# Kernel optimization log

Hardware: AMD Instinct MI355X
Metric: run time of the kernel (lower is better)

The kernel has to match this reference:

```python
import jax, jax.numpy as jnp
import numpy as np

# ---- config mirrored from FullyFusedNGP.__init__ (scale=1) ----
SCALE = 1.0
L, F, LOG2_T, N_MIN = 16, 2, 19, 16
T = 1 << LOG2_T  # 524288 entries per level
B = float(np.exp(np.log(2048.0 * SCALE / N_MIN) / (L - 1)))  # per_level_scale
RES = np.array([int(np.ceil(N_MIN * B**l - 1.0)) + 1 for l in range(L)], dtype=np.int32)
PRIMES = np.array([1, 2654435761, 805459861], dtype=np.uint32)  # tcnn hash primes
CORNERS = np.array([[(i >> k) & 1 for k in range(3)] for i in range(8)], dtype=np.int32)  # [8,3]
N_PTS = 262144


def hash_encode(xn, table):
    """Multi-resolution hash grid with trilinear interpolation.
    xn: [N,3] in [0,1]; table: [L,T,F] -> returns [N, L*F]."""
    res = jnp.asarray(RES)
    corners = jnp.asarray(CORNERS)
    pos = xn[None] * (res[:, None, None] - 1).astype(xn.dtype)        # [L,N,3]
    p0 = jnp.floor(pos).astype(jnp.int32)
    w = pos - p0                                                      # [L,N,3] trilinear fracs
    idx = p0[:, :, None, :] + corners[None, None]                     # [L,N,8,3]
    idx = jnp.clip(idx, 0, (res - 1)[:, None, None, None])
    ui = idx.astype(jnp.uint32)
    h = (ui[..., 0] * PRIMES[0]) ^ (ui[..., 1] * PRIMES[1]) ^ (ui[..., 2] * PRIMES[2])
    h = (h & jnp.uint32(T - 1)).astype(jnp.int32)                     # [L,N,8]
    feats = jax.vmap(lambda t, hh: t[hh])(table, h)                   # [L,N,8,F] gather
    cw = jnp.where(corners[None, None].astype(bool),
                   w[:, :, None, :], 1.0 - w[:, :, None, :]).prod(-1)  # [L,N,8]
    feat = (feats * cw[..., None]).sum(2)                             # [L,N,F]
    return jnp.moveaxis(feat, 0, 1).reshape(xn.shape[0], L * F)       # [N,32]


def sh_encode(d01):
    """Spherical harmonics degree 4 (tcnn convention, input in [0,1]). [N,3]->[N,16]."""
    d = 2.0 * d01 - 1.0
    x, y, z = d[:, 0], d[:, 1], d[:, 2]
    xy, xz, yz = x * y, x * z, y * z
    x2, y2, z2 = x * x, y * y, z * z
    return jnp.stack([
        jnp.full_like(x, 0.28209479177387814),
        -0.48860251190291987 * y,
        0.48860251190291987 * z,
        -0.48860251190291987 * x,
        1.0925484305920792 * xy,
        -1.0925484305920792 * yz,
        0.94617469575755997 * z2 - 0.31539156525251999,
        -1.0925484305920792 * xz,
        0.54627421529603959 * (x2 - y2),
        0.59004358992664352 * y * (-3.0 * x2 + y2),
        2.8906114426405538 * xy * z,
        0.45704579946446572 * y * (1.0 - 5.0 * z2),
        0.3731763325901154 * z * (5.0 * z2 - 3.0),
        0.45704579946446572 * x * (1.0 - 5.0 * z2),
        1.4453057213202769 * z * (x2 - y2),
        0.59004358992664352 * x * (-x2 + 3.0 * y2),
    ], axis=1)


def setup_inputs() -> dict:
    key = jax.random.key(0)
    ks = jax.random.split(key, 8)
    x = jax.random.uniform(ks[0], (N_PTS, 3), jnp.float32, -SCALE, SCALE)
    d = jax.random.normal(ks[1], (N_PTS, 3), jnp.float32)
    d = d / jnp.linalg.norm(d, axis=1, keepdims=True)
    table = jax.random.uniform(ks[2], (L, T, F), jnp.float32, -1e-4, 1e-4)
    def w(k, fi, fo):  # bias-free FullyFusedMLP weights
        return jax.random.normal(k, (fi, fo), jnp.float32) * (1.0 / np.sqrt(fi))
    return {
        'x': x, 'd': d, 'table': table,
        'w1': w(ks[3], 32, 64), 'w2': w(ks[4], 64, 16),
        'w_in': w(ks[5], 32, 64), 'w_h': w(ks[6], 64, 64), 'w_out': w(ks[7], 64, 3),
    }


def reference(x, d, table, w1, w2, w_in, w_h, w_out):
    xn = (x + SCALE) / (2.0 * SCALE)                 # (x - xyz_min)/(xyz_max - xyz_min)
    enc = hash_encode(xn, table)                     # [N,32]
    h = jax.nn.relu(enc @ w1) @ w2                   # density MLP, 1 hidden layer -> [N,16]
    sigmas = jnp.exp(h[:, 0])                        # TruncExp forward == exp
    sh = sh_encode((d + 1.0) * 0.5)                  # [N,16]
    a = jax.nn.relu(jnp.concatenate([sh, h], axis=1) @ w_in)
    a = jax.nn.relu(a @ w_h)
    rgbs = jax.nn.sigmoid(a @ w_out)                 # [N,3]
    return sigmas, rgbs
```

## Files before the change

kernel.cpp:

```cpp
#include <hip/hip_runtime.h>
#include <hip/hip_bf16.h>
#include <stdint.h>

typedef __bf16 bf16x8 __attribute__((ext_vector_type(8)));
typedef float  f32x4  __attribute__((ext_vector_type(4)));

__device__ __forceinline__ int imin(int a, int b) { return a < b ? a : b; }
__device__ __forceinline__ int imax(int a, int b) { return a > b ? a : b; }

#define TMASK ((1u << 19) - 1u)

__constant__ int cRES[16] = {16, 23, 31, 43, 59, 81, 112, 154,
                             213, 295, 407, 562, 777, 1073, 1483, 2048};

__global__ void __launch_bounds__(256) ngp_encode(
    const float* __restrict__ xin,
    const float2* __restrict__ tab,
    float2* __restrict__ enc,
    int n, int lbase)
{
    const int bid = blockIdx.x;
    const int l = lbase + (bid & 7);
    const int p = (bid >> 3) * 256 + threadIdx.x;
    if (p >= n) return;

    const int rm = cRES[l] - 1;
    const float rf = (float)rm;

    const float xn0 = (xin[3 * p + 0] + 1.0f) * 0.5f;
    const float xn1 = (xin[3 * p + 1] + 1.0f) * 0.5f;
    const float xn2 = (xin[3 * p + 2] + 1.0f) * 0.5f;

    const float p0 = xn0 * rf, p1 = xn1 * rf, p2 = xn2 * rf;
    const float f0 = floorf(p0), f1 = floorf(p1), f2 = floorf(p2);
    const int i0 = (int)f0, i1 = (int)f1, i2 = (int)f2;
    const float w0 = p0 - f0, w1 = p1 - f1, w2 = p2 - f2;

    const int a0 = imax(imin(i0, rm), 0), b0 = imax(imin(i0 + 1, rm), 0);
    const int a1 = imax(imin(i1, rm), 0), b1 = imax(imin(i1 + 1, rm), 0);
    const int a2 = imax(imin(i2, rm), 0), b2 = imax(imin(i2 + 1, rm), 0);

    const uint32_t t0a = (uint32_t)a0;
    const uint32_t t0b = (uint32_t)b0;
    const uint32_t t1a = (uint32_t)a1 * 2654435761u;
    const uint32_t t1b = (uint32_t)b1 * 2654435761u;
    const uint32_t t2a = (uint32_t)a2 * 805459861u;
    const uint32_t t2b = (uint32_t)b2 * 805459861u;
    const uint32_t base = (uint32_t)l << 19;

    const float2 v000 = tab[base + ((t0a ^ t1a ^ t2a) & TMASK)];
    const float2 v100 = tab[base + ((t0b ^ t1a ^ t2a) & TMASK)];
    const float2 v010 = tab[base + ((t0a ^ t1b ^ t2a) & TMASK)];
    const float2 v110 = tab[base + ((t0b ^ t1b ^ t2a) & TMASK)];
    const float2 v001 = tab[base + ((t0a ^ t1a ^ t2b) & TMASK)];
    const float2 v101 = tab[base + ((t0b ^ t1a ^ t2b) & TMASK)];
    const float2 v011 = tab[base + ((t0a ^ t1b ^ t2b) & TMASK)];
    const float2 v111 = tab[base + ((t0b ^ t1b ^ t2b) & TMASK)];

    const float u0 = 1.0f - w0, u1 = 1.0f - w1, u2 = 1.0f - w2;
    float e0 = 0.0f, e1 = 0.0f;
    {   float cw = u0 * u1 * u2;  e0 = fmaf(v000.x, cw, e0); e1 = fmaf(v000.y, cw, e1); }
    {   float cw = w0 * u1 * u2;  e0 = fmaf(v100.x, cw, e0); e1 = fmaf(v100.y, cw, e1); }
    {   float cw = u0 * w1 * u2;  e0 = fmaf(v010.x, cw, e0); e1 = fmaf(v010.y, cw, e1); }
    {   float cw = w0 * w1 * u2;  e0 = fmaf(v110.x, cw, e0); e1 = fmaf(v110.y, cw, e1); }
    {   float cw = u0 * u1 * w2;  e0 = fmaf(v001.x, cw, e0); e1 = fmaf(v001.y, cw, e1); }
    {   float cw = w0 * u1 * w2;  e0 = fmaf(v101.x, cw, e0); e1 = fmaf(v101.y, cw, e1); }
    {   float cw = u0 * w1 * w2;  e0 = fmaf(v011.x, cw, e0); e1 = fmaf(v011.y, cw, e1); }
    {   float cw = w0 * w1 * w2;  e0 = fmaf(v111.x, cw, e0); e1 = fmaf(v111.y, cw, e1); }

    union { double d; float2 f; } u;
    u.f = make_float2(e0, e1);
    __builtin_nontemporal_store(u.d, (double*)&enc[(size_t)l * n + p]);
}

__global__ void __launch_bounds__(256) ngp_mlp_mfma(
    const float2* __restrict__ enc,
    const float* __restrict__ din,
    const float* __restrict__ W1,
    const float* __restrict__ W2,
    const float* __restrict__ WIN,
    const float* __restrict__ WH,
    const float* __restrict__ WOUT,
    float* __restrict__ out,
    int n, int ntiles)
{
    __shared__ float lds[4][16 * 68];
    const int tid  = threadIdx.x;
    const int wid  = tid >> 6;
    const int lane = tid & 63;
    const int c = lane & 15;
    const int g = lane >> 4;
    float* buf = &lds[wid][0];

    bf16x8 w1f[4], w2f[2], winf[4], whf[2][4], woutf[2];
    #pragma unroll
    for (int n4 = 0; n4 < 4; ++n4)
        #pragma unroll
        for (int j = 0; j < 8; ++j)
            w1f[n4][j] = (__bf16)W1[(g * 8 + j) * 64 + n4 * 16 + c];
    #pragma unroll
    for (int kc = 0; kc < 2; ++kc)
        #pragma unroll
        for (int j = 0; j < 8; ++j)
            w2f[kc][j] = (__bf16)W2[(kc * 32 + g * 8 + j) * 16 + c];
    #pragma unroll
    for (int n4 = 0; n4 < 4; ++n4)
        #pragma unroll
        for (int j = 0; j < 8; ++j)
            winf[n4][j] = (__bf16)WIN[(g * 8 + j) * 64 + n4 * 16 + c];
    #pragma unroll
    for (int kc = 0; kc < 2; ++kc)
        #pragma unroll
        for (int n4 = 0; n4 < 4; ++n4)
            #pragma unroll
            for (int j = 0; j < 8; ++j)
                whf[kc][n4][j] = (__bf16)WH[(kc * 32 + g * 8 + j) * 64 + n4 * 16 + c];
    #pragma unroll
    for (int kc = 0; kc < 2; ++kc)
        #pragma unroll
        for (int j = 0; j < 8; ++j)
            woutf[kc][j] = (c < 3) ? (__bf16)WOUT[(kc * 32 + g * 8 + j) * 3 + c]
                                   : (__bf16)0.0f;

    for (int t = blockIdx.x; t < ntiles; t += gridDim.x) {
        const int pbase = t * 64 + wid * 16;
        const int pc = pbase + c;

        bf16x8 a1;
        #pragma unroll
        for (int m = 0; m < 4; ++m) {
            const float2 e = enc[(size_t)(4 * g + m) * n + pc];
            a1[2 * m]     = (__bf16)e.x;
            a1[2 * m + 1] = (__bf16)e.y;
        }

        #pragma unroll
        for (int n4 = 0; n4 < 4; ++n4) {
            f32x4 d = {0.f, 0.f, 0.f, 0.f};
            d = __builtin_amdgcn_mfma_f32_16x16x32_bf16(a1, w1f[n4], d, 0, 0, 0);
            #pragma unroll
            for (int r = 0; r < 4; ++r)
                buf[(g * 4 + r) * 68 + n4 * 16 + c] = fmaxf(d[r], 0.0f);
        }

        f32x4 hacc = {0.f, 0.f, 0.f, 0.f};
        #pragma unroll
        for (int kc = 0; kc < 2; ++kc) {
            bf16x8 a2;
            const float* src = &buf[c * 68 + kc * 32 + g * 8];
            #pragma unroll
            for (int j = 0; j < 8; ++j) a2[j] = (__bf16)src[j];
            hacc = __builtin_amdgcn_mfma_f32_16x16x32_bf16(a2, w2f[kc], hacc, 0, 0, 0);
        }

        if (c == 0) {
            #pragma unroll
            for (int r = 0; r < 4; ++r)
                out[pbase + g * 4 + r] = __expf(hacc[r]);
        }

        #pragma unroll
        for (int r = 0; r < 4; ++r)
            buf[(g * 4 + r) * 68 + c] = hacc[r];

        const float dx = din[3 * pc + 0];
        const float dy = din[3 * pc + 1];
        const float dz = din[3 * pc + 2];
        const float xy = dx * dy, xz = dx * dz, yz = dy * dz;
        const float x2 = dx * dx, y2 = dy * dy, z2 = dz * dz;
        float shv[16];
        shv[0]  = 0.28209479177387814f;
        shv[1]  = -0.48860251190291987f * dy;
        shv[2]  = 0.48860251190291987f * dz;
        shv[3]  = -0.48860251190291987f * dx;
        shv[4]  = 1.0925484305920792f * xy;
        shv[5]  = -1.0925484305920792f * yz;
        shv[6]  = 0.94617469575756f * z2 - 0.31539156525252f;
        shv[7]  = -1.0925484305920792f * xz;
        shv[8]  = 0.5462742152960396f * (x2 - y2);
        shv[9]  = 0.5900435899266435f * dy * (-3.0f * x2 + y2);
        shv[10] = 2.890611442640554f * xy * dz;
        shv[11] = 0.4570457994644657f * dy * (1.0f - 5.0f * z2);
        shv[12] = 0.3731763325901154f * dz * (5.0f * z2 - 3.0f);
        shv[13] = 0.4570457994644657f * dx * (1.0f - 5.0f * z2);
        shv[14] = 1.445305721320277f * dz * (x2 - y2);
        shv[15] = 0.5900435899266435f * dx * (-x2 + 3.0f * y2);

        bf16x8 a3;
        if (g < 2) {
            #pragma unroll
            for (int j = 0; j < 8; ++j) a3[j] = (__bf16)shv[g * 8 + j];
        } else {
            const float* hsrc = &buf[c * 68 + (g - 2) * 8];
            #pragma unroll
            for (int j = 0; j < 8; ++j) a3[j] = (__bf16)hsrc[j];
        }

        #pragma unroll
        for (int n4 = 0; n4 < 4; ++n4) {
            f32x4 d = {0.f, 0.f, 0.f, 0.f};
            d = __builtin_amdgcn_mfma_f32_16x16x32_bf16(a3, winf[n4], d, 0, 0, 0);
            #pragma unroll
            for (int r = 0; r < 4; ++r)
                buf[(g * 4 + r) * 68 + n4 * 16 + c] = fmaxf(d[r], 0.0f);
        }

        bf16x8 a4[2];
        #pragma unroll
        for (int kc = 0; kc < 2; ++kc) {
            const float* src = &buf[c * 68 + kc * 32 + g * 8];
            #pragma unroll
            for (int j = 0; j < 8; ++j) a4[kc][j] = (__bf16)src[j];
        }
        f32x4 d4[4];
        #pragma unroll
        for (int n4 = 0; n4 < 4; ++n4) d4[n4] = (f32x4){0.f, 0.f, 0.f, 0.f};
        #pragma unroll
        for (int kc = 0; kc < 2; ++kc)
            #pragma unroll
            for (int n4 = 0; n4 < 4; ++n4)
                d4[n4] = __builtin_amdgcn_mfma_f32_16x16x32_bf16(a4[kc], whf[kc][n4], d4[n4], 0, 0, 0);
        #pragma unroll
        for (int n4 = 0; n4 < 4; ++n4)
            #pragma unroll
            for (int r = 0; r < 4; ++r)
                buf[(g * 4 + r) * 68 + n4 * 16 + c] = fmaxf(d4[n4][r], 0.0f);

        f32x4 d5 = {0.f, 0.f, 0.f, 0.f};
        #pragma unroll
        for (int kc = 0; kc < 2; ++kc) {
            bf16x8 a5;
            const float* src = &buf[c * 68 + kc * 32 + g * 8];
            #pragma unroll
            for (int j = 0; j < 8; ++j) a5[j] = (__bf16)src[j];
            d5 = __builtin_amdgcn_mfma_f32_16x16x32_bf16(a5, woutf[kc], d5, 0, 0, 0);
        }
        if (c < 3) {
            #pragma unroll
            for (int r = 0; r < 4; ++r)
                out[n + 3 * (pbase + g * 4 + r) + c] = 1.0f / (1.0f + __expf(-d5[r]));
        }
    }
}

__global__ void __launch_bounds__(256) ngp_mlp(
    const float2* __restrict__ enc, const float* __restrict__ din,
    const float* __restrict__ W1, const float* __restrict__ W2,
    const float* __restrict__ WIN, const float* __restrict__ WH,
    const float* __restrict__ WOUT, float* __restrict__ out, int n)
{
    const int i = blockIdx.x * 256 + threadIdx.x;
    if (i >= n) return;
    float h1[64];
    #pragma unroll
    for (int j = 0; j < 64; ++j) h1[j] = 0.0f;
    #pragma unroll
    for (int l = 0; l < 16; ++l) {
        const float2 e = enc[(size_t)l * n + i];
        #pragma unroll
        for (int j = 0; j < 64; ++j)
            h1[j] = fmaf(e.x, W1[(2 * l) * 64 + j], fmaf(e.y, W1[(2 * l + 1) * 64 + j], h1[j]));
    }
    float h[16];
    #pragma unroll
    for (int j = 0; j < 16; ++j) h[j] = 0.0f;
    #pragma unroll
    for (int k = 0; k < 64; ++k) {
        const float v = fmaxf(h1[k], 0.0f);
        #pragma unroll
        for (int j = 0; j < 16; ++j) h[j] = fmaf(v, W2[k * 16 + j], h[j]);
    }
    out[i] = __expf(h[0]);
    const float dx = din[3 * i + 0], dy = din[3 * i + 1], dz = din[3 * i + 2];
    const float xy = dx * dy, xz = dx * dz, yz = dy * dz;
    const float x2 = dx * dx, y2 = dy * dy, z2 = dz * dz;
    float sh[16];
    sh[0]  = 0.28209479177387814f;
    sh[1]  = -0.48860251190291987f * dy;
    sh[2]  = 0.48860251190291987f * dz;
    sh[3]  = -0.48860251190291987f * dx;
    sh[4]  = 1.0925484305920792f * xy;
    sh[5]  = -1.0925484305920792f * yz;
    sh[6]  = 0.94617469575756f * z2 - 0.31539156525252f;
    sh[7]  = -1.0925484305920792f * xz;
    sh[8]  = 0.5462742152960396f * (x2 - y2);
    sh[9]  = 0.5900435899266435f * dy * (-3.0f * x2 + y2);
    sh[10] = 2.890611442640554f * xy * dz;
    sh[11] = 0.4570457994644657f * dy * (1.0f - 5.0f * z2);
    sh[12] = 0.3731763325901154f * dz * (5.0f * z2 - 3.0f);
    sh[13] = 0.4570457994644657f * dx * (1.0f - 5.0f * z2);
    sh[14] = 1.445305721320277f * dz * (x2 - y2);
    sh[15] = 0.5900435899266435f * dx * (-x2 + 3.0f * y2);
    float av[64];
    #pragma unroll
    for (int j = 0; j < 64; ++j) av[j] = 0.0f;
    #pragma unroll
    for (int k = 0; k < 16; ++k) {
        const float v = sh[k];
        #pragma unroll
        for (int j = 0; j < 64; ++j) av[j] = fmaf(v, WIN[k * 64 + j], av[j]);
    }
    #pragma unroll
    for (int k = 0; k < 16; ++k) {
        const float v = h[k];
        #pragma unroll
        for (int j = 0; j < 64; ++j) av[j] = fmaf(v, WIN[(16 + k) * 64 + j], av[j]);
    }
    float bv[64];
    #pragma unroll
    for (int j = 0; j < 64; ++j) bv[j] = 0.0f;
    #pragma unroll
    for (int k = 0; k < 64; ++k) {
        const float v = fmaxf(av[k], 0.0f);
        #pragma unroll
        for (int j = 0; j < 64; ++j) bv[j] = fmaf(v, WH[k * 64 + j], bv[j]);
    }
    float r0 = 0.0f, r1 = 0.0f, r2 = 0.0f;
    #pragma unroll
    for (int k = 0; k < 64; ++k) {
        const float v = fmaxf(bv[k], 0.0f);
        r0 = fmaf(v, WOUT[k * 3 + 0], r0);
        r1 = fmaf(v, WOUT[k * 3 + 1], r1);
        r2 = fmaf(v, WOUT[k * 3 + 2], r2);
    }
    out[n + 3 * i + 0] = 1.0f / (1.0f + __expf(-r0));
    out[n + 3 * i + 1] = 1.0f / (1.0f + __expf(-r1));
    out[n + 3 * i + 2] = 1.0f / (1.0f + __expf(-r2));
}

extern "C" void kernel_launch(void* const* d_in, const int* in_sizes, int n_in,
                              void* d_out, int out_size, void* d_ws, size_t ws_size,
                              hipStream_t stream)
{
    const float* x    = (const float*)d_in[0];
    const float* d    = (const float*)d_in[1];
    const float* tb   = (const float*)d_in[2];
    const float* w1   = (const float*)d_in[3];
    const float* w2   = (const float*)d_in[4];
    const float* win  = (const float*)d_in[5];
    const float* wh   = (const float*)d_in[6];
    const float* wout = (const float*)d_in[7];

    const int n = in_sizes[0] / 3;
    const size_t enc_bytes = (size_t)16 * n * sizeof(float2);
    float2* enc = (float2*)d_ws;

    ngp_encode<<<(n / 256) * 8, 256, 0, stream>>>(x, (const float2*)tb, enc, n, 0);
    ngp_encode<<<(n / 256) * 8, 256, 0, stream>>>(x, (const float2*)tb, enc, n, 8);

    if (ws_size >= enc_bytes) {
        const int ntiles = n / 64;
        ngp_mlp_mfma<<<512, 256, 0, stream>>>(enc, d, w1, w2, win, wh, wout,
                                              (float*)d_out, n, ntiles);
    } else {
        ngp_mlp<<<n / 256, 256, 0, stream>>>(enc, d, w1, w2, win, wh, wout,
                                             (float*)d_out, n);
    }
}
```

Before: 249.2 us.

## Process four points per thread in one 16-level encode launch, widen MLP grid

Merges the two 8-level encode launches into a single launch covering all 16 levels. Each thread now handles four points and issues all 32 hash-table gathers before any interpolation, to expose more memory-level parallelism. The x loads become nontemporal, and the MLP kernel grid goes from 512 to 1024 blocks. The cost is higher register pressure from holding 32 float2 values per thread, which may lower occupancy. The bounds check is dropped, so n must be a multiple of 1024.

```diff
diff --git a/kernel.cpp b/kernel.cpp
--- a/kernel.cpp
+++ b/kernel.cpp
@@ -13,64 +13,85 @@
 __constant__ int cRES[16] = {16, 23, 31, 43, 59, 81, 112, 154,
                              213, 295, 407, 562, 777, 1073, 1483, 2048};
 
-__global__ void __launch_bounds__(256) ngp_encode(
+__global__ void __launch_bounds__(256) ngp_encode4(
     const float* __restrict__ xin,
     const float2* __restrict__ tab,
     float2* __restrict__ enc,
-    int n, int lbase)
+    int n)
 {
     const int bid = blockIdx.x;
-    const int l = lbase + (bid & 7);
-    const int p = (bid >> 3) * 256 + threadIdx.x;
-    if (p >= n) return;
+    const int l = bid & 15;
+    const int pblk = (bid >> 4) * 1024 + threadIdx.x;
 
     const int rm = cRES[l] - 1;
     const float rf = (float)rm;
-
-    const float xn0 = (xin[3 * p + 0] + 1.0f) * 0.5f;
-    const float xn1 = (xin[3 * p + 1] + 1.0f) * 0.5f;
-    const float xn2 = (xin[3 * p + 2] + 1.0f) * 0.5f;
-
-    const float p0 = xn0 * rf, p1 = xn1 * rf, p2 = xn2 * rf;
-    const float f0 = floorf(p0), f1 = floorf(p1), f2 = floorf(p2);
-    const int i0 = (int)f0, i1 = (int)f1, i2 = (int)f2;
-    const float w0 = p0 - f0, w1 = p1 - f1, w2 = p2 - f2;
-
-    const int a0 = imax(imin(i0, rm), 0), b0 = imax(imin(i0 + 1, rm), 0);
-    const int a1 = imax(imin(i1, rm), 0), b1 = imax(imin(i1 + 1, rm), 0);
-    const int a2 = imax(imin(i2, rm), 0), b2 = imax(imin(i2 + 1, rm), 0);
-
-    const uint32_t t0a = (uint32_t)a0;
-    const uint32_t t0b = (uint32_t)b0;
-    const uint32_t t1a = (uint32_t)a1 * 2654435761u;
-    const uint32_t t1b = (uint32_t)b1 * 2654435761u;
-    const uint32_t t2a = (uint32_t)a2 * 805459861u;
-    const uint32_t t2b = (uint32_t)b2 * 805459861u;
     const uint32_t base = (uint32_t)l << 19;
 
-    const float2 v000 = tab[base + ((t0a ^ t1a ^ t2a) & TMASK)];
-    const float2 v100 = tab[base + ((t0b ^ t1a ^ t2a) & TMASK)];
-    const float2 v010 = tab[base + ((t0a ^ t1b ^ t2a) & TMASK)];
-    const float2 v110 = tab[base + ((t0b ^ t1b ^ t2a) & TMASK)];
-    const float2 v001 = tab[base + ((t0a ^ t1a ^ t2b) & TMASK)];
-    const float2 v101 = tab[base + ((t0b ^ t1a ^ t2b) & TMASK)];
-    const float2 v011 = tab[base + ((t0a ^ t1b ^ t2b) & TMASK)];
-    const float2 v111 = tab[base + ((t0b ^ t1b ^ t2b) & TMASK)];
-
-    const float u0 = 1.0f - w0, u1 = 1.0f - w1, u2 = 1.0f - w2;
-    float e0 = 0.0f, e1 = 0.0f;
-    {   float cw = u0 * u1 * u2;  e0 = fmaf(v000.x, cw, e0); e1 = fmaf(v000.y, cw, e1); }
-    {   float cw = w0 * u1 * u2;  e0 = fmaf(v100.x, cw, e0); e1 = fmaf(v100.y, cw, e1); }
-    {   float cw = u0 * w1 * u2;  e0 = fmaf(v010.x, cw, e0); e1 = fmaf(v010.y, cw, e1); }
-    {   float cw = w0 * w1 * u2;  e0 = fmaf(v110.x, cw, e0); e1 = fmaf(v110.y, cw, e1); }
-    {   float cw = u0 * u1 * w2;  e0 = fmaf(v001.x, cw, e0); e1 = fmaf(v001.y, cw, e1); }
-    {   float cw = w0 * u1 * w2;  e0 = fmaf(v101.x, cw, e0); e1 = fmaf(v101.y, cw, e1); }
-    {   float cw = u0 * w1 * w2;  e0 = fmaf(v011.x, cw, e0); e1 = fmaf(v011.y, cw, e1); }
-    {   float cw = w0 * w1 * w2;  e0 = fmaf(v111.x, cw, e0); e1 = fmaf(v111.y, cw, e1); }
-
-    union { double d; float2 f; } u;
-    u.f = make_float2(e0, e1);
-    __builtin_nontemporal_store(u.d, (double*)&enc[(size_t)l * n + p]);
+    uint32_t idx[4][8];
+    float wa[4][3];
+
+    #pragma unroll
+    for (int q = 0; q < 4; ++q) {
+        const int p = pblk + q * 256;
+        const float x0 = __builtin_nontemporal_load(&xin[3 * p + 0]);
+        const float x1 = __builtin_nontemporal_load(&xin[3 * p + 1]);
+        const float x2 = __builtin_nontemporal_load(&xin[3 * p + 2]);
+        const float xn0 = (x0 + 1.0f) * 0.5f;
+        const float xn1 = (x1 + 1.0f) * 0.5f;
+        const float xn2 = (x2 + 1.0f) * 0.5f;
+
+        const float p0 = xn0 * rf, p1 = xn1 * rf, p2 = xn2 * rf;
+        const float f0 = floorf(p0), f1 = floorf(p1), f2 = floorf(p2);
+        const int i0 = (int)f0, i1 = (int)f1, i2 = (int)f2;
+        wa[q][0] = p0 - f0; wa[q][1] = p1 - f1; wa[q][2] = p2 - f2;
+
+        const int a0 = imax(imin(i0, rm), 0), b0 = imax(imin(i0 + 1, rm), 0);
+        const int a1 = imax(imin(i1, rm), 0), b1 = imax(imin(i1 + 1, rm), 0);
+        const int a2 = imax(imin(i2, rm), 0), b2 = imax(imin(i2 + 1, rm), 0);
+
+        const uint32_t t0a = (uint32_t)a0;
+        const uint32_t t0b = (uint32_t)b0;
+        const uint32_t t1a = (uint32_t)a1 * 2654435761u;
+        const uint32_t t1b = (uint32_t)b1 * 2654435761u;
+        const uint32_t t2a = (uint32_t)a2 * 805459861u;
+        const uint32_t t2b = (uint32_t)b2 * 805459861u;
+
+        idx[q][0] = base + ((t0a ^ t1a ^ t2a) & TMASK);
+        idx[q][1] = base + ((t0b ^ t1a ^ t2a) & TMASK);
+        idx[q][2] = base + ((t0a ^ t1b ^ t2a) & TMASK);
+        idx[q][3] = base + ((t0b ^ t1b ^ t2a) & TMASK);
+        idx[q][4] = base + ((t0a ^ t1a ^ t2b) & TMASK);
+        idx[q][5] = base + ((t0b ^ t1a ^ t2b) & TMASK);
+        idx[q][6] = base + ((t0a ^ t1b ^ t2b) & TMASK);
+        idx[q][7] = base + ((t0b ^ t1b ^ t2b) & TMASK);
+    }
+
+    float2 v[4][8];
+    #pragma unroll
+    for (int q = 0; q < 4; ++q)
+        #pragma unroll
+        for (int cor = 0; cor < 8; ++cor)
+            v[q][cor] = tab[idx[q][cor]];
+
+    #pragma unroll
+    for (int q = 0; q < 4; ++q) {
+        const float w0 = wa[q][0], w1 = wa[q][1], w2 = wa[q][2];
+        const float u0 = 1.0f - w0, u1 = 1.0f - w1, u2 = 1.0f - w2;
+        float e0 = 0.0f, e1 = 0.0f;
+        {   float cw = u0 * u1 * u2;  e0 = fmaf(v[q][0].x, cw, e0); e1 = fmaf(v[q][0].y, cw, e1); }
+        {   float cw = w0 * u1 * u2;  e0 = fmaf(v[q][1].x, cw, e0); e1 = fmaf(v[q][1].y, cw, e1); }
+        {   float cw = u0 * w1 * u2;  e0 = fmaf(v[q][2].x, cw, e0); e1 = fmaf(v[q][2].y, cw, e1); }
+        {   float cw = w0 * w1 * u2;  e0 = fmaf(v[q][3].x, cw, e0); e1 = fmaf(v[q][3].y, cw, e1); }
+        {   float cw = u0 * u1 * w2;  e0 = fmaf(v[q][4].x, cw, e0); e1 = fmaf(v[q][4].y, cw, e1); }
+        {   float cw = w0 * u1 * w2;  e0 = fmaf(v[q][5].x, cw, e0); e1 = fmaf(v[q][5].y, cw, e1); }
+        {   float cw = u0 * w1 * w2;  e0 = fmaf(v[q][6].x, cw, e0); e1 = fmaf(v[q][6].y, cw, e1); }
+        {   float cw = w0 * w1 * w2;  e0 = fmaf(v[q][7].x, cw, e0); e1 = fmaf(v[q][7].y, cw, e1); }
+
+        union { double d; float2 f; } u;
+        u.f = make_float2(e0, e1);
+        const int p = pblk + q * 256;
+        __builtin_nontemporal_store(u.d, (double*)&enc[(size_t)l * n + p]);
+    }
 }
 
 __global__ void __launch_bounds__(256) ngp_mlp_mfma(
@@ -345,13 +366,12 @@
     const size_t enc_bytes = (size_t)16 * n * sizeof(float2);
     float2* enc = (float2*)d_ws;
 
-    ngp_encode<<<(n / 256) * 8, 256, 0, stream>>>(x, (const float2*)tb, enc, n, 0);
-    ngp_encode<<<(n / 256) * 8, 256, 0, stream>>>(x, (const float2*)tb, enc, n, 8);
+    ngp_encode4<<<(n / 1024) * 16, 256, 0, stream>>>(x, (const float2*)tb, enc, n);
 
     if (ws_size >= enc_bytes) {
         const int ntiles = n / 64;
-        ngp_mlp_mfma<<<512, 256, 0, stream>>>(enc, d, w1, w2, win, wh, wout,
-                                              (float*)d_out, n, ntiles);
+        ngp_mlp_mfma<<<1024, 256, 0, stream>>>(enc, d, w1, w2, win, wh, wout,
+                                               (float*)d_out, n, ntiles);
     } else {
         ngp_mlp<<<n / 256, 256, 0, stream>>>(enc, d, w1, w2, win, wh, wout,
                                              (float*)d_out, n);
```

Result: slower. 283.9 us (+13.9%).

## Fuse hash encoding into MFMA MLP kernel and prepack weight fragments

Applied to the files above, without the earlier changes.

The separate hash-encode kernels and the MLP kernel are merged into one kernel. Each lane gathers the 32 corner entries for its 4 levels directly into the MFMA A-fragment, so the 32 MB encoding intermediate is never written to or read from global memory. A small prep kernel converts the weights once into bf16 MFMA fragment layout, and every block then loads them with vector loads instead of converting them per block. Each block now handles one tile rather than looping persistently. The cost is higher register pressure from 32 outstanding gathers per lane, and the weight fragments are reloaded per block.

```diff
diff --git a/kernel.cpp b/kernel.cpp
--- a/kernel.cpp
+++ b/kernel.cpp
@@ -13,76 +13,56 @@
 __constant__ int cRES[16] = {16, 23, 31, 43, 59, 81, 112, 154,
                              213, 295, 407, 562, 777, 1073, 1483, 2048};
 
-__global__ void __launch_bounds__(256) ngp_encode(
+__global__ void __launch_bounds__(64) prep_wfrag(
+    const float* __restrict__ W1, const float* __restrict__ W2,
+    const float* __restrict__ WIN, const float* __restrict__ WH,
+    const float* __restrict__ WOUT, uint4* __restrict__ wf)
+{
+    const int lane = threadIdx.x;
+    const int c = lane & 15, g = lane >> 4;
+    bf16x8 f;
+    #pragma unroll
+    for (int n4 = 0; n4 < 4; ++n4) {
+        #pragma unroll
+        for (int j = 0; j < 8; ++j) f[j] = (__bf16)W1[(g * 8 + j) * 64 + n4 * 16 + c];
+        wf[n4 * 64 + lane] = *reinterpret_cast<uint4*>(&f);
+    }
+    #pragma unroll
+    for (int kc = 0; kc < 2; ++kc) {
+        #pragma unroll
+        for (int j = 0; j < 8; ++j) f[j] = (__bf16)W2[(kc * 32 + g * 8 + j) * 16 + c];
+        wf[(4 + kc) * 64 + lane] = *reinterpret_cast<uint4*>(&f);
+    }
+    #pragma unroll
+    for (int n4 = 0; n4 < 4; ++n4) {
+        #pragma unroll
+        for (int j = 0; j < 8; ++j) f[j] = (__bf16)WIN[(g * 8 + j) * 64 + n4 * 16 + c];
+        wf[(6 + n4) * 64 + lane] = *reinterpret_cast<uint4*>(&f);
+    }
+    #pragma unroll
+    for (int kc = 0; kc < 2; ++kc)
+        #pragma unroll
+        for (int n4 = 0; n4 < 4; ++n4) {
+            #pragma unroll
+            for (int j = 0; j < 8; ++j) f[j] = (__bf16)WH[(kc * 32 + g * 8 + j) * 64 + n4 * 16 + c];
+            wf[(10 + kc * 4 + n4) * 64 + lane] = *reinterpret_cast<uint4*>(&f);
+        }
+    #pragma unroll
+    for (int kc = 0; kc < 2; ++kc) {
+        #pragma unroll
+        for (int j = 0; j < 8; ++j)
+            f[j] = (c < 3) ? (__bf16)WOUT[(kc * 32 + g * 8 + j) * 3 + c] : (__bf16)0.0f;
+        wf[(18 + kc) * 64 + lane] = *reinterpret_cast<uint4*>(&f);
+    }
+}
+
+__global__ void __launch_bounds__(256) ngp_fused(
     const float* __restrict__ xin,
+    const float* __restrict__ din,
     const float2* __restrict__ tab,
-    float2* __restrict__ enc,
-    int n, int lbase)
-{
-    const int bid = blockIdx.x;
-    const int l = lbase + (bid & 7);
-    const int p = (bid >> 3) * 256 + threadIdx.x;
-    if (p >= n) return;
-
-    const int rm = cRES[l] - 1;
-    const float rf = (float)rm;
-
-    const float xn0 = (xin[3 * p + 0] + 1.0f) * 0.5f;
-    const float xn1 = (xin[3 * p + 1] + 1.0f) * 0.5f;
-    const float xn2 = (xin[3 * p + 2] + 1.0f) * 0.5f;
-
-    const float p0 = xn0 * rf, p1 = xn1 * rf, p2 = xn2 * rf;
-    const float f0 = floorf(p0), f1 = floorf(p1), f2 = floorf(p2);
-    const int i0 = (int)f0, i1 = (int)f1, i2 = (int)f2;
-    const float w0 = p0 - f0, w1 = p1 - f1, w2 = p2 - f2;
-
-    const int a0 = imax(imin(i0, rm), 0), b0 = imax(imin(i0 + 1, rm), 0);
-    const int a1 = imax(imin(i1, rm), 0), b1 = imax(imin(i1 + 1, rm), 0);
-    const int a2 = imax(imin(i2, rm), 0), b2 = imax(imin(i2 + 1, rm), 0);
-
-    const uint32_t t0a = (uint32_t)a0;
-    const uint32_t t0b = (uint32_t)b0;
-    const uint32_t t1a = (uint32_t)a1 * 2654435761u;
-    const uint32_t t1b = (uint32_t)b1 * 2654435761u;
-    const uint32_t t2a = (uint32_t)a2 * 805459861u;
-    const uint32_t t2b = (uint32_t)b2 * 805459861u;
-    const uint32_t base = (uint32_t)l << 19;
-
-    const float2 v000 = tab[base + ((t0a ^ t1a ^ t2a) & TMASK)];
-    const float2 v100 = tab[base + ((t0b ^ t1a ^ t2a) & TMASK)];
-    const float2 v010 = tab[base + ((t0a ^ t1b ^ t2a) & TMASK)];
-    const float2 v110 = tab[base + ((t0b ^ t1b ^ t2a) & TMASK)];
-    const float2 v001 = tab[base + ((t0a ^ t1a ^ t2b) & TMASK)];
-    const float2 v101 = tab[base + ((t0b ^ t1a ^ t2b) & TMASK)];
-    const float2 v011 = tab[base + ((t0a ^ t1b ^ t2b) & TMASK)];
-    const float2 v111 = tab[base + ((t0b ^ t1b ^ t2b) & TMASK)];
-
-    const float u0 = 1.0f - w0, u1 = 1.0f - w1, u2 = 1.0f - w2;
-    float e0 = 0.0f, e1 = 0.0f;
-    {   float cw = u0 * u1 * u2;  e0 = fmaf(v000.x, cw, e0); e1 = fmaf(v000.y, cw, e1); }
-    {   float cw = w0 * u1 * u2;  e0 = fmaf(v100.x, cw, e0); e1 = fmaf(v100.y, cw, e1); }
-    {   float cw = u0 * w1 * u2;  e0 = fmaf(v010.x, cw, e0); e1 = fmaf(v010.y, cw, e1); }
-    {   float cw = w0 * w1 * u2;  e0 = fmaf(v110.x, cw, e0); e1 = fmaf(v110.y, cw, e1); }
-    {   float cw = u0 * u1 * w2;  e0 = fmaf(v001.x, cw, e0); e1 = fmaf(v001.y, cw, e1); }
-    {   float cw = w0 * u1 * w2;  e0 = fmaf(v101.x, cw, e0); e1 = fmaf(v101.y, cw, e1); }
-    {   float cw = u0 * w1 * w2;  e0 = fmaf(v011.x, cw, e0); e1 = fmaf(v011.y, cw, e1); }
-    {   float cw = w0 * w1 * w2;  e0 = fmaf(v111.x, cw, e0); e1 = fmaf(v111.y, cw, e1); }
-
-    union { double d; float2 f; } u;
-    u.f = make_float2(e0, e1);
-    __builtin_nontemporal_store(u.d, (double*)&enc[(size_t)l * n + p]);
-}
-
-__global__ void __launch_bounds__(256) ngp_mlp_mfma(
-    const float2* __restrict__ enc,
-    const float* __restrict__ din,
-    const float* __restrict__ W1,
-    const float* __restrict__ W2,
-    const float* __restrict__ WIN,
-    const float* __restrict__ WH,
-    const float* __restrict__ WOUT,
+    const uint4* __restrict__ wf,
     float* __restrict__ out,
-    int n, int ntiles)
+    int n)
 {
     __shared__ float lds[4][16 * 68];
     const int tid  = threadIdx.x;
@@ -91,241 +71,197 @@
     const int c = lane & 15;
     const int g = lane >> 4;
     float* buf = &lds[wid][0];
-
+    const int pbase = blockIdx.x * 64 + wid * 16;
+    const int pc = pbase + c;
+
+    const float xn0 = (xin[3 * pc + 0] + 1.0f) * 0.5f;
+    const float xn1 = (xin[3 * pc + 1] + 1.0f) * 0.5f;
+    const float xn2 = (xin[3 * pc + 2] + 1.0f) * 0.5f;
+
+    uint32_t idx[4][8];
+    float wa[4][3];
+    #pragma unroll
+    for (int m = 0; m < 4; ++m) {
+        const int lv = 4 * g + m;
+        const int rm = cRES[lv] - 1;
+        const float rf = (float)rm;
+        const uint32_t base = (uint32_t)lv << 19;
+
+        const float p0 = xn0 * rf, p1 = xn1 * rf, p2 = xn2 * rf;
+        const float f0 = floorf(p0), f1 = floorf(p1), f2 = floorf(p2);
+        const int i0 = (int)f0, i1 = (int)f1, i2 = (int)f2;
+        wa[m][0] = p0 - f0; wa[m][1] = p1 - f1; wa[m][2] = p2 - f2;
+
+        const int a0 = imax(imin(i0, rm), 0), b0 = imax(imin(i0 + 1, rm), 0);
+        const int a1i = imax(imin(i1, rm), 0), b1 = imax(imin(i1 + 1, rm), 0);
+        const int a2 = imax(imin(i2, rm), 0), b2 = imax(imin(i2 + 1, rm), 0);
+
+        const uint32_t t0a = (uint32_t)a0;
+        const uint32_t t0b = (uint32_t)b0;
+        const uint32_t t1a = (uint32_t)a1i * 2654435761u;
+        const uint32_t t1b = (uint32_t)b1 * 2654435761u;
+        const uint32_t t2a = (uint32_t)a2 * 805459861u;
+        const uint32_t t2b = (uint32_t)b2 * 805459861u;
+
+        idx[m][0] = base + ((t0a ^ t1a ^ t2a) & TMASK);
+        idx[m][1] = base + ((t0b ^ t1a ^ t2a) & TMASK);
+        idx[m][2] = base + ((t0a ^ t1b ^ t2a) & TMASK);
+        idx[m][3] = base + ((t0b ^ t1b ^ t2a) & TMASK);
+        idx[m][4] = base + ((t0a ^ t1a ^ t2b) & TMASK);
+        idx[m][5] = base + ((t0b ^ t1a ^ t2b) & TMASK);
+        idx[m][6] = base + ((t0a ^ t1b ^ t2b) & TMASK);
+        idx[m][7] = base + ((t0b ^ t1b ^ t2b) & TMASK);
+    }
+
+    float2 v[4][8];
+    #pragma unroll
+    for (int m = 0; m < 4; ++m)
+        #pragma unroll
+        for (int cor = 0; cor < 8; ++cor)
+            v[m][cor] = tab[idx[m][cor]];
+
+    __builtin_amdgcn_sched_barrier(0);
+
+    bf16x8 a1;
+    #pragma unroll
+    for (int m = 0; m < 4; ++m) {
+        const float w0 = wa[m][0], w1 = wa[m][1], w2 = wa[m][2];
+        const float u0 = 1.0f - w0, u1 = 1.0f - w1, u2 = 1.0f - w2;
+        float e0 = 0.0f, e1 = 0.0f;
+        {   float cw = u0 * u1 * u2;  e0 = fmaf(v[m][0].x, cw, e0); e1 = fmaf(v[m][0].y, cw, e1); }
+        {   float cw = w0 * u1 * u2;  e0 = fmaf(v[m][1].x, cw, e0); e1 = fmaf(v[m][1].y, cw, e1); }
+        {   float cw = u0 * w1 * u2;  e0 = fmaf(v[m][2].x, cw, e0); e1 = fmaf(v[m][2].y, cw, e1); }
+        {   float cw = w0 * w1 * u2;  e0 = fmaf(v[m][3].x, cw, e0); e1 = fmaf(v[m][3].y, cw, e1); }
+        {   float cw = u0 * u1 * w2;  e0 = fmaf(v[m][4].x, cw, e0); e1 = fmaf(v[m][4].y, cw, e1); }
+        {   float cw = w0 * u1 * w2;  e0 = fmaf(v[m][5].x, cw, e0); e1 = fmaf(v[m][5].y, cw, e1); }
+        {   float cw = u0 * w1 * w2;  e0 = fmaf(v[m][6].x, cw, e0); e1 = fmaf(v[m][6].y, cw, e1); }
+        {   float cw = w0 * w1 * w2;  e0 = fmaf(v[m][7].x, cw, e0); e1 = fmaf(v[m][7].y, cw, e1); }
+        a1[2 * m]     = (__bf16)e0;
+        a1[2 * m + 1] = (__bf16)e1;
+    }
+
+    #define LDW(f_) (*reinterpret_cast<const bf16x8*>(&wf[(f_) * 64 + lane]))
     bf16x8 w1f[4], w2f[2], winf[4], whf[2][4], woutf[2];
     #pragma unroll
-    for (int n4 = 0; n4 < 4; ++n4)
-        #pragma unroll
-        for (int j = 0; j < 8; ++j)
-            w1f[n4][j] = (__bf16)W1[(g * 8 + j) * 64 + n4 * 16 + c];
+    for (int n4 = 0; n4 < 4; ++n4) w1f[n4] = LDW(n4);
+    #pragma unroll
+    for (int kc = 0; kc < 2; ++kc) w2f[kc] = LDW(4 + kc);
+    #pragma unroll
+    for (int n4 = 0; n4 < 4; ++n4) winf[n4] = LDW(6 + n4);
     #pragma unroll
     for (int kc = 0; kc < 2; ++kc)
         #pragma unroll
-        for (int j = 0; j < 8; ++j)
-            w2f[kc][j] = (__bf16)W2[(kc * 32 + g * 8 + j) * 16 + c];
-    #pragma unroll
-    for (int n4 = 0; n4 < 4; ++n4)
-        #pragma unroll
-        for (int j = 0; j < 8; ++j)
-            winf[n4][j] = (__bf16)WIN[(g * 8 + j) * 64 + n4 * 16 + c];
-    #pragma unroll
-    for (int kc = 0; kc < 2; ++kc)
-        #pragma unroll
-        for (int n4 = 0; n4 < 4; ++n4)
-            #pragma unroll
-            for (int j = 0; j < 8; ++j)
-                whf[kc][n4][j] = (__bf16)WH[(kc * 32 + g * 8 + j) * 64 + n4 * 16 + c];
-    #pragma unroll
-    for (int kc = 0; kc < 2; ++kc)
-        #pragma unroll
-        for (int j = 0; j < 8; ++j)
-            woutf[kc][j] = (c < 3) ? (__bf16)WOUT[(kc * 32 + g * 8 + j) * 3 + c]
-                                   : (__bf16)0.0f;
-
-    for (int t = blockIdx.x; t < ntiles; t += gridDim.x) {
-        const int pbase = t * 64 + wid * 16;
-        const int pc = pbase + c;
-
-        bf16x8 a1;
-        #pragma unroll
-        for (int m = 0; m < 4; ++m) {
-            const float2 e = enc[(size_t)(4 * g + m) * n + pc];
-            a1[2 * m]     = (__bf16)e.x;
-            a1[2 * m + 1] = (__bf16)e.y;
-        }
-
-        #pragma unroll
-        for (int n4 = 0; n4 < 4; ++n4) {
-            f32x4 d = {0.f, 0.f, 0.f, 0.f};
-            d = __builtin_amdgcn_mfma_f32_16x16x32_bf16(a1, w1f[n4], d, 0, 0, 0);
-            #pragma unroll
-            for (int r = 0; r < 4; ++r)
-                buf[(g * 4 + r) * 68 + n4 * 16 + c] = fmaxf(d[r], 0.0f);
-        }
-
-        f32x4 hacc = {0.f, 0.f, 0.f, 0.f};
-        #pragma unroll
-        for (int kc = 0; kc < 2; ++kc) {
-            bf16x8 a2;
-            const float* src = &buf[c * 68 + kc * 32 + g * 8];
-            #pragma unroll
-            for (int j = 0; j < 8; ++j) a2[j] = (__bf16)src[j];
-            hacc = __builtin_amdgcn_mfma_f32_16x16x32_bf16(a2, w2f[kc], hacc, 0, 0, 0);
-        }
-
-        if (c == 0) {
-            #pragma unroll
-            for (int r = 0; r < 4; ++r)
-                out[pbase + g * 4 + r] = __expf(hacc[r]);
-        }
-
-        #pragma unroll
-        for (int r = 0; r < 4; ++r)
-            buf[(g * 4 + r) * 68 + c] = hacc[r];
-
-        const float dx = din[3 * pc + 0];
-        const float dy = din[3 * pc + 1];
-        const float dz = din[3 * pc + 2];
-        const float xy = dx * dy, xz = dx * dz, yz = dy * dz;
-        const float x2 = dx * dx, y2 = dy * dy, z2 = dz * dz;
-        float shv[16];
-        shv[0]  = 0.28209479177387814f;
-        shv[1]  = -0.48860251190291987f * dy;
-        shv[2]  = 0.48860251190291987f * dz;
-        shv[3]  = -0.48860251190291987f * dx;
-        shv[4]  = 1.0925484305920792f * xy;
-        shv[5]  = -1.0925484305920792f * yz;
-        shv[6]  = 0.94617469575756f * z2 - 0.31539156525252f;
-        shv[7]  = -1.0925484305920792f * xz;
-        shv[8]  = 0.5462742152960396f * (x2 - y2);
-        shv[9]  = 0.5900435899266435f * dy * (-3.0f * x2 + y2);
-        shv[10] = 2.890611442640554f * xy * dz;
-        shv[11] = 0.4570457994644657f * dy * (1.0f - 5.0f * z2);
-        shv[12] = 0.3731763325901154f * dz * (5.0f * z2 - 3.0f);
-        shv[13] = 0.4570457994644657f * dx * (1.0f - 5.0f * z2);
-        shv[14] = 1.445305721320277f * dz * (x2 - y2);
-        shv[15] = 0.5900435899266435f * dx * (-x2 + 3.0f * y2);
-
-        bf16x8 a3;
-        if (g < 2) {
-            #pragma unroll
-            for (int j = 0; j < 8; ++j) a3[j] = (__bf16)shv[g * 8 + j];
-        } else {
-            const float* hsrc = &buf[c * 68 + (g - 2) * 8];
-            #pragma unroll
-            for (int j = 0; j < 8; ++j) a3[j] = (__bf16)hsrc[j];
-        }
-
-        #pragma unroll
-        for (int n4 = 0; n4 < 4; ++n4) {
-            f32x4 d = {0.f, 0.f, 0.f, 0.f};
-            d = __builtin_amdgcn_mfma_f32_16x16x32_bf16(a3, winf[n4], d, 0, 0, 0);
-            #pragma unroll
-            for (int r = 0; r < 4; ++r)
-                buf[(g * 4 + r) * 68 + n4 * 16 + c] = fmaxf(d[r], 0.0f);
-        }
-
-        bf16x8 a4[2];
-        #pragma unroll
-        for (int kc = 0; kc < 2; ++kc) {
-            const float* src = &buf[c * 68 + kc * 32 + g * 8];
-            #pragma unroll
-            for (int j = 0; j < 8; ++j) a4[kc][j] = (__bf16)src[j];
-        }
-        f32x4 d4[4];
-        #pragma unroll
-        for (int n4 = 0; n4 < 4; ++n4) d4[n4] = (f32x4){0.f, 0.f, 0.f, 0.f};
-        #pragma unroll
-        for (int kc = 0; kc < 2; ++kc)
-            #pragma unroll
-            for (int n4 = 0; n4 < 4; ++n4)
-                d4[n4] = __builtin_amdgcn_mfma_f32_16x16x32_bf16(a4[kc], whf[kc][n4], d4[n4], 0, 0, 0);
-        #pragma unroll
-        for (int n4 = 0; n4 < 4; ++n4)
-            #pragma unroll
-            for (int r = 0; r < 4; ++r)
-                buf[(g * 4 + r) * 68 + n4 * 16 + c] = fmaxf(d4[n4][r], 0.0f);
-
-        f32x4 d5 = {0.f, 0.f, 0.f, 0.f};
-        #pragma unroll
-        for (int kc = 0; kc < 2; ++kc) {
-            bf16x8 a5;
-            const float* src = &buf[c * 68 + kc * 32 + g * 8];
-            #pragma unroll
-            for (int j = 0; j < 8; ++j) a5[j] = (__bf16)src[j];
-            d5 = __builtin_amdgcn_mfma_f32_16x16x32_bf16(a5, woutf[kc], d5, 0, 0, 0);
-        }
-        if (c < 3) {
-            #pragma unroll
-            for (int r = 0; r < 4; ++r)
-                out[n + 3 * (pbase + g * 4 + r) + c] = 1.0f / (1.0f + __expf(-d5[r]));
-        }
-    }
-}
-
-__global__ void __launch_bounds__(256) ngp_mlp(
-    const float2* __restrict__ enc, const float* __restrict__ din,
-    const float* __restrict__ W1, const float* __restrict__ W2,
-    const float* __restrict__ WIN, const float* __restrict__ WH,
-    const float* __restrict__ WOUT, float* __restrict__ out, int n)
-{
-    const int i = blockIdx.x * 256 + threadIdx.x;
-    if (i >= n) return;
-    float h1[64];
-    #pragma unroll
-    for (int j = 0; j < 64; ++j) h1[j] = 0.0f;
-    #pragma unroll
-    for (int l = 0; l < 16; ++l) {
-        const float2 e = enc[(size_t)l * n + i];
-        #pragma unroll
-        for (int j = 0; j < 64; ++j)
-            h1[j] = fmaf(e.x, W1[(2 * l) * 64 + j], fmaf(e.y, W1[(2 * l + 1) * 64 + j], h1[j]));
-    }
-    float h[16];
-    #pragma unroll
-    for (int j = 0; j < 16; ++j) h[j] = 0.0f;
-    #pragma unroll
-    for (int k = 0; k < 64; ++k) {
-        const float v = fmaxf(h1[k], 0.0f);
-        #pragma unroll
-        for (int j = 0; j < 16; ++j) h[j] = fmaf(v, W2[k * 16 + j], h[j]);
-    }
-    out[i] = __expf(h[0]);
-    const float dx = din[3 * i + 0], dy = din[3 * i + 1], dz = din[3 * i + 2];
+        for (int n4 = 0; n4 < 4; ++n4) whf[kc][n4] = LDW(10 + kc * 4 + n4);
+    #pragma unroll
+    for (int kc = 0; kc < 2; ++kc) woutf[kc] = LDW(18 + kc);
+    #undef LDW
+
+    #pragma unroll
+    for (int n4 = 0; n4 < 4; ++n4) {
+        f32x4 d = {0.f, 0.f, 0.f, 0.f};
+        d = __builtin_amdgcn_mfma_f32_16x16x32_bf16(a1, w1f[n4], d, 0, 0, 0);
+        #pragma unroll
+        for (int r = 0; r < 4; ++r)
+            buf[(g * 4 + r) * 68 + n4 * 16 + c] = fmaxf(d[r], 0.0f);
+    }
+
+    f32x4 hacc = {0.f, 0.f, 0.f, 0.f};
+    #pragma unroll
+    for (int kc = 0; kc < 2; ++kc) {
+        bf16x8 a2;
+        const float* src = &buf[c * 68 + kc * 32 + g * 8];
+        #pragma unroll
+        for (int j = 0; j < 8; ++j) a2[j] = (__bf16)src[j];
+        hacc = __builtin_amdgcn_mfma_f32_16x16x32_bf16(a2, w2f[kc], hacc, 0, 0, 0);
+    }
+
+    if (c == 0) {
+        #pragma unroll
+        for (int r = 0; r < 4; ++r)
+            out[pbase + g * 4 + r] = __expf(hacc[r]);
+    }
+
+    #pragma unroll
+    for (int r = 0; r < 4; ++r)
+        buf[(g * 4 + r) * 68 + c] = hacc[r];
+
+    const float dx = din[3 * pc + 0];
+    const float dy = din[3 * pc + 1];
+    const float dz = din[3 * pc + 2];
     const float xy = dx * dy, xz = dx * dz, yz = dy * dz;
     const float x2 = dx * dx, y2 = dy * dy, z2 = dz * dz;
-    float sh[16];
-    sh[0]  = 0.28209479177387814f;
-    sh[1]  = -0.48860251190291987f * dy;
-    sh[2]  = 0.48860251190291987f * dz;
-    sh[3]  = -0.48860251190291987f * dx;
-    sh[4]  = 1.0925484305920792f * xy;
-    sh[5]  = -1.0925484305920792f * yz;
-    sh[6]  = 0.94617469575756f * z2 - 0.31539156525252f;
-    sh[7]  = -1.0925484305920792f * xz;
-    sh[8]  = 0.5462742152960396f * (x2 - y2);
-    sh[9]  = 0.5900435899266435f * dy * (-3.0f * x2 + y2);
-    sh[10] = 2.890611442640554f * xy * dz;
-    sh[11] = 0.4570457994644657f * dy * (1.0f - 5.0f * z2);
-    sh[12] = 0.3731763325901154f * dz * (5.0f * z2 - 3.0f);
-    sh[13] = 0.4570457994644657f * dx * (1.0f - 5.0f * z2);
-    sh[14] = 1.445305721320277f * dz * (x2 - y2);
-    sh[15] = 0.5900435899266435f * dx * (-x2 + 3.0f * y2);
-    float av[64];
-    #pragma unroll
-    for (int j = 0; j < 64; ++j) av[j] = 0.0f;
-    #pragma unroll
-    for (int k = 0; k < 16; ++k) {
-        const float v = sh[k];
-        #pragma unroll
-        for (int j = 0; j < 64; ++j) av[j] = fmaf(v, WIN[k * 64 + j], av[j]);
-    }
-    #pragma unroll
-    for (int k = 0; k < 16; ++k) {
-        const float v = h[k];
-        #pragma unroll
-        for (int j = 0; j < 64; ++j) av[j] = fmaf(v, WIN[(16 + k) * 64 + j], av[j]);
-    }
-    float bv[64];
-    #pragma unroll
-    for (int j = 0; j < 64; ++j) bv[j] = 0.0f;
-    #pragma unroll
-    for (int k = 0; k < 64; ++k) {
-        const float v = fmaxf(av[k], 0.0f);
-        #pragma unroll
-        for (int j = 0; j < 64; ++j) bv[j] = fmaf(v, WH[k * 64 + j], bv[j]);
-    }
-    float r0 = 0.0f, r1 = 0.0f, r2 = 0.0f;
-    #pragma unroll
-    for (int k = 0; k < 64; ++k) {
-        const float v = fmaxf(bv[k], 0.0f);
-        r0 = fmaf(v, WOUT[k * 3 + 0], r0);
-        r1 = fmaf(v, WOUT[k * 3 + 1], r1);
-        r2 = fmaf(v, WOUT[k * 3 + 2], r2);
-    }
-    out[n + 3 * i + 0] = 1.0f / (1.0f + __expf(-r0));
-    out[n + 3 * i + 1] = 1.0f / (1.0f + __expf(-r1));
-    out[n + 3 * i + 2] = 1.0f / (1.0f + __expf(-r2));
+    float shv[16];
+    shv[0]  = 0.28209479177387814f;
+    shv[1]  = -0.48860251190291987f * dy;
+    shv[2]  = 0.48860251190291987f * dz;
+    shv[3]  = -0.48860251190291987f * dx;
+    shv[4]  = 1.0925484305920792f * xy;
+    shv[5]  = -1.0925484305920792f * yz;
+    shv[6]  = 0.94617469575756f * z2 - 0.31539156525252f;
+    shv[7]  = -1.0925484305920792f * xz;
+    shv[8]  = 0.5462742152960396f * (x2 - y2);
+    shv[9]  = 0.5900435899266435f * dy * (-3.0f * x2 + y2);
+    shv[10] = 2.890611442640554f * xy * dz;
+    shv[11] = 0.4570457994644657f * dy * (1.0f - 5.0f * z2);
+    shv[12] = 0.3731763325901154f * dz * (5.0f * z2 - 3.0f);
+    shv[13] = 0.4570457994644657f * dx * (1.0f - 5.0f * z2);
+    shv[14] = 1.445305721320277f * dz * (x2 - y2);
+    shv[15] = 0.5900435899266435f * dx * (-x2 + 3.0f * y2);
+
+    bf16x8 a3;
+    if (g < 2) {
+        #pragma unroll
+        for (int j = 0; j < 8; ++j) a3[j] = (__bf16)shv[g * 8 + j];
+    } else {
+        const float* hsrc = &buf[c * 68 + (g - 2) * 8];
+        #pragma unroll
+        for (int j = 0; j < 8; ++j) a3[j] = (__bf16)hsrc[j];
+    }
+
+    #pragma unroll
+    for (int n4 = 0; n4 < 4; ++n4) {
+        f32x4 d = {0.f, 0.f, 0.f, 0.f};
+        d = __builtin_amdgcn_mfma_f32_16x16x32_bf16(a3, winf[n4], d, 0, 0, 0);
+        #pragma unroll
+        for (int r = 0; r < 4; ++r)
+            buf[(g * 4 + r) * 68 + n4 * 16 + c] = fmaxf(d[r], 0.0f);
+    }
+
+    bf16x8 a4[2];
+    #pragma unroll
+    for (int kc = 0; kc < 2; ++kc) {
+        const float* src = &buf[c * 68 + kc * 32 + g * 8];
+        #pragma unroll
+        for (int j = 0; j < 8; ++j) a4[kc][j] = (__bf16)src[j];
+    }
+    f32x4 d4[4];
+    #pragma unroll
+    for (int n4 = 0; n4 < 4; ++n4) d4[n4] = (f32x4){0.f, 0.f, 0.f, 0.f};
+    #pragma unroll
+    for (int kc = 0; kc < 2; ++kc)
+        #pragma unroll
+        for (int n4 = 0; n4 < 4; ++n4)
+            d4[n4] = __builtin_amdgcn_mfma_f32_16x16x32_bf16(a4[kc], whf[kc][n4], d4[n4], 0, 0, 0);
+    #pragma unroll
+    for (int n4 = 0; n4 < 4; ++n4)
+        #pragma unroll
+        for (int r = 0; r < 4; ++r)
+            buf[(g * 4 + r) * 68 + n4 * 16 + c] = fmaxf(d4[n4][r], 0.0f);
+
+    f32x4 d5 = {0.f, 0.f, 0.f, 0.f};
+    #pragma unroll
+    for (int kc = 0; kc < 2; ++kc) {
+        bf16x8 a5;
+        const float* src = &buf[c * 68 + kc * 32 + g * 8];
+        #pragma unroll
+        for (int j = 0; j < 8; ++j) a5[j] = (__bf16)src[j];
+        d5 = __builtin_amdgcn_mfma_f32_16x16x32_bf16(a5, woutf[kc], d5, 0, 0, 0);
+    }
+    if (c < 3) {
+        #pragma unroll
+        for (int r = 0; r < 4; ++r)
+            out[n + 3 * (pbase + g * 4 + r) + c] = 1.0f / (1.0f + __expf(-d5[r]));
+    }
 }
 
 extern "C" void kernel_launch(void* const* d_in, const int* in_sizes, int n_in,
@@ -342,18 +278,9 @@
     const float* wout = (const float*)d_in[7];
 
     const int n = in_sizes[0] / 3;
-    const size_t enc_bytes = (size_t)16 * n * sizeof(float2);
-    float2* enc = (float2*)d_ws;
-
-    ngp_encode<<<(n / 256) * 8, 256, 0, stream>>>(x, (const float2*)tb, enc, n, 0);
-    ngp_encode<<<(n / 256) * 8, 256, 0, stream>>>(x, (const float2*)tb, enc, n, 8);
-
-    if (ws_size >= enc_bytes) {
-        const int ntiles = n / 64;
-        ngp_mlp_mfma<<<512, 256, 0, stream>>>(enc, d, w1, w2, win, wh, wout,
-                                              (float*)d_out, n, ntiles);
-    } else {
-        ngp_mlp<<<n / 256, 256, 0, stream>>>(enc, d, w1, w2, win, wh, wout,
-                                             (float*)d_out, n);
-    }
+    uint4* wf = (uint4*)d_ws;
+
+    prep_wfrag<<<1, 64, 0, stream>>>(w1, w2, win, wh, wout, wf);
+    ngp_fused<<<n / 64, 256, 0, stream>>>(x, d, (const float2*)tb, wf,
+                                          (float*)d_out, n);
 }
```

Measured after the change: 327.4 us. 31.4% more time.
